# Kernel optimization log

Measured on AMD Instinct MI355X. Metric: run time of the kernel, lower is better.

## Reference

```python
import jax, jax.numpy as jnp
import numpy as np

D_INNER = 5120
DT_RANK = 160
N_STATE = 16
BATCH = 256


def _softplus_thresh20(x):
    # ttnn.softplus(parameter1=1.0, parameter2=20.0): linear above threshold 20
    return jnp.where(x > 20.0, x, jnp.log1p(jnp.exp(jnp.minimum(x, 20.0))))


def setup_inputs() -> dict:
    key = jax.random.key(0)
    ks = jax.random.split(key, 9)
    x = jax.random.normal(ks[0], (1, 1, BATCH, D_INNER), dtype=jnp.float32)
    # scale weights by 1/sqrt(fan_in) so softplus input is O(1)
    W_dt_low = jax.random.normal(ks[1], (D_INNER, DT_RANK), dtype=jnp.float32) / np.sqrt(D_INNER)
    W_dt = jax.random.normal(ks[2], (DT_RANK, D_INNER), dtype=jnp.float32) / np.sqrt(DT_RANK)
    b_dt = jax.random.normal(ks[3], (D_INNER,), dtype=jnp.float32)
    W_B = jax.random.normal(ks[4], (D_INNER, N_STATE), dtype=jnp.float32) / np.sqrt(D_INNER)
    W_C = jax.random.normal(ks[5], (D_INNER, N_STATE), dtype=jnp.float32) / np.sqrt(D_INNER)
    # A = -exp(A_log): strictly negative, as in the module's preprocess_A
    A = -jnp.exp(0.5 * jax.random.normal(ks[6], (D_INNER, N_STATE), dtype=jnp.float32))
    D = jax.random.normal(ks[7], (D_INNER,), dtype=jnp.float32)
    h0 = 0.1 * jax.random.normal(ks[8], (BATCH, D_INNER, N_STATE), dtype=jnp.float32)
    return {"x": x, "W_dt_low": W_dt_low, "W_dt": W_dt, "b_dt": b_dt,
            "W_B": W_B, "W_C": W_C, "A": A, "D": D, "h0": h0}


def reference(x, W_dt_low, W_dt, b_dt, W_B, W_C, A, D, h0):
    b, d = x.shape[2], x.shape[3]
    xb = x.reshape(b, d)                                  # (B, D)
    # delta = softplus(x @ x_proj_dt @ dt_proj + bias)
    delta = _softplus_thresh20(xb @ W_dt_low @ W_dt + b_dt)   # (B, D)
    Bp = xb @ W_B                                         # (B, N)
    Cp = xb @ W_C                                         # (B, N)
    # discretize: abar = exp(delta * A), bbar = delta * B
    # layout (B, D, N) matches repeat_interleave(delta, n) / repeat(B, d)
    abar = jnp.exp(delta[:, :, None] * A[None, :, :])     # (B, D, N)
    bbar = delta[:, :, None] * Bp[:, None, :]             # (B, D, N)
    h = abar * h0 + bbar * xb[:, :, None]                 # (B, D, N)
    y = jnp.einsum('bdn,bn->bd', h, Cp)                   # reduce over state
    out = xb * D[None, :] + y                             # (B, D)
    return out.reshape(1, 1, b, d)
```

## Files before the change

kernel.cpp:

```cpp
#include <hip/hip_runtime.h>
#include <math.h>

#define D_INNER 5120
#define DT_RANK 160
#define N_STATE 16
#define BATCH   256
#define KTOT    192

#define BGRP    8
#define NBG     (BATCH / BGRP)
#define DDBLK   160
#define NDDB    (D_INNER / DDBLK)
#define SPLIT   32

#define OFF_T     0
#define SZ_T      (BATCH * KTOT)
#define OFF_P     (OFF_T + SZ_T)
#define SZ_P      (SPLIT * BATCH * KTOT)
#define OFF_DELTA OFF_P

__global__ __launch_bounds__(256) void k1_gemm(const float* __restrict__ x,
                                               const float* __restrict__ Wdtlow,
                                               const float* __restrict__ WB,
                                               const float* __restrict__ WC,
                                               float* __restrict__ ws) {
    __shared__ float lds[4 * BGRP * KTOT];
    const int tid  = threadIdx.x;
    const int lane = tid & 63;
    const int wv   = tid >> 6;
    const int b0   = blockIdx.x * BGRP;
    const int ddB  = blockIdx.y * DDBLK;

    float* xs = lds;
    for (int j = tid; j < (BGRP * DDBLK) / 4; j += 256) {
        int i  = j / (DDBLK / 4);
        int c4 = j % (DDBLK / 4);
        float4 v = *(const float4*)(x + (size_t)(b0 + i) * D_INNER + ddB + c4 * 4);
        *(float4*)(xs + i * DDBLK + c4 * 4) = v;
    }
    __syncthreads();

    const int dd0 = wv * 40;
    const float* p0 = Wdtlow + (size_t)(ddB + dd0) * DT_RANK + lane;
    const float* p1 = p0 + 64;
    const float* p2;
    int st2;
    if (lane < 32)      { p2 = p0 + 128;                                          st2 = DT_RANK; }
    else if (lane < 48) { p2 = WB + (size_t)(ddB + dd0) * N_STATE + (lane - 32);  st2 = N_STATE; }
    else                { p2 = WC + (size_t)(ddB + dd0) * N_STATE + (lane - 48);  st2 = N_STATE; }

    float acc0[BGRP], acc1[BGRP], acc2[BGRP];
#pragma unroll
    for (int i = 0; i < BGRP; ++i) { acc0[i] = 0.f; acc1[i] = 0.f; acc2[i] = 0.f; }

#pragma unroll 2
    for (int g = 0; g < 10; ++g) {
        float w0[4], w1[4], w2[4];
#pragma unroll
        for (int u = 0; u < 4; ++u) {
            int dd = g * 4 + u;
            w0[u] = p0[(size_t)dd * DT_RANK];
            w1[u] = p1[(size_t)dd * DT_RANK];
            w2[u] = p2[(size_t)dd * st2];
        }
#pragma unroll
        for (int i = 0; i < BGRP; ++i) {
            float4 xv = *(const float4*)(xs + i * DDBLK + dd0 + g * 4);
            acc0[i] += xv.x * w0[0] + xv.y * w0[1] + xv.z * w0[2] + xv.w * w0[3];
            acc1[i] += xv.x * w1[0] + xv.y * w1[1] + xv.z * w1[2] + xv.w * w1[3];
            acc2[i] += xv.x * w2[0] + xv.y * w2[1] + xv.z * w2[2] + xv.w * w2[3];
        }
    }
    __syncthreads();

#pragma unroll
    for (int i = 0; i < BGRP; ++i) {
        float* r = lds + wv * (BGRP * KTOT) + i * KTOT;
        r[lane]       = acc0[i];
        r[lane + 64]  = acc1[i];
        r[lane + 128] = acc2[i];
    }
    __syncthreads();

    float* P = ws + OFF_P + (size_t)blockIdx.y * (BATCH * KTOT) + (size_t)b0 * KTOT;
#pragma unroll
    for (int r = 0; r < 6; ++r) {
        int idx = tid + r * 256;
        float v = lds[idx] + lds[idx + 1536] + lds[idx + 3072] + lds[idx + 4608];
        P[idx] = v;
    }
}

__global__ __launch_bounds__(256) void k2_reduce(float* __restrict__ ws) {
    int g = blockIdx.x * 256 + threadIdx.x;
    const float* P = ws + OFF_P;
    float a = 0.f;
#pragma unroll
    for (int s = 0; s < SPLIT; ++s) a += P[(size_t)s * (BATCH * KTOT) + g];
    ws[OFF_T + g] = a;
}

#define K3A_BT 8
__global__ __launch_bounds__(256) void k3a_delta(const float* __restrict__ Wdt,
                                                 const float* __restrict__ b_dt,
                                                 float* __restrict__ ws) {
    __shared__ float ts[DT_RANK * K3A_BT];
    const int tid = threadIdx.x;
    const int d   = blockIdx.x * 256 + tid;
    const int b0  = blockIdx.y * K3A_BT;
    const float* T = ws + OFF_T;

    for (int j = tid; j < DT_RANK * K3A_BT; j += 256) {
        int b = j & (K3A_BT - 1);
        int k = j >> 3;
        ts[j] = T[(size_t)(b0 + b) * KTOT + k];
    }
    __syncthreads();

    float acc[K3A_BT];
#pragma unroll
    for (int i = 0; i < K3A_BT; ++i) acc[i] = 0.f;

#pragma unroll 4
    for (int k = 0; k < DT_RANK; ++k) {
        float w = Wdt[(size_t)k * D_INNER + d];
        float4 t0 = *(const float4*)(ts + k * 8);
        float4 t1 = *(const float4*)(ts + k * 8 + 4);
        acc[0] += t0.x * w; acc[1] += t0.y * w; acc[2] += t0.z * w; acc[3] += t0.w * w;
        acc[4] += t1.x * w; acc[5] += t1.y * w; acc[6] += t1.z * w; acc[7] += t1.w * w;
    }

    const float bv = b_dt[d];
    float* delta = ws + OFF_DELTA;
#pragma unroll
    for (int i = 0; i < K3A_BT; ++i) {
        float v  = acc[i] + bv;
        float dl = (v > 20.f) ? v : log1pf(__expf(v));
        delta[(size_t)(b0 + i) * D_INNER + d] = dl;
    }
}

__global__ __launch_bounds__(256) void k3b_scan(const float* __restrict__ x,
                                                const float* __restrict__ A,
                                                const float* __restrict__ Dv,
                                                const float* __restrict__ h0,
                                                const float* __restrict__ ws,
                                                float* __restrict__ out) {
    const int tid  = threadIdx.x;
    const int dsub = tid >> 2;
    const int nq   = tid & 3;
    const int d    = blockIdx.x * 64 + dsub;
    const int b    = blockIdx.y;

    const float* Tb = ws + OFF_T + (size_t)b * KTOT;
    float sbc = 0.f;
#pragma unroll
    for (int n = 0; n < N_STATE; ++n) sbc += Tb[160 + n] * Tb[176 + n];
    float cp0 = Tb[176 + nq * 4 + 0];
    float cp1 = Tb[176 + nq * 4 + 1];
    float cp2 = Tb[176 + nq * 4 + 2];
    float cp3 = Tb[176 + nq * 4 + 3];

    const float delta = ws[OFF_DELTA + (size_t)b * D_INNER + d];
    float4 a = ((const float4*)(A + (size_t)d * N_STATE))[nq];
    float4 h = ((const float4*)(h0 + ((size_t)b * D_INNER + d) * N_STATE))[nq];

    float y = __expf(delta * a.x) * h.x * cp0
            + __expf(delta * a.y) * h.y * cp1
            + __expf(delta * a.z) * h.z * cp2
            + __expf(delta * a.w) * h.w * cp3;
    y += __shfl_xor(y, 1);
    y += __shfl_xor(y, 2);

    if (nq == 0) {
        float xv = x[(size_t)b * D_INNER + d];
        out[(size_t)b * D_INNER + d] = xv * (Dv[d] + delta * sbc) + y;
    }
}

extern "C" void kernel_launch(void* const* d_in, const int* in_sizes, int n_in,
                              void* d_out, int out_size, void* d_ws, size_t ws_size,
                              hipStream_t stream) {
    const float* x      = (const float*)d_in[0];
    const float* Wdtlow = (const float*)d_in[1];
    const float* Wdt    = (const float*)d_in[2];
    const float* bdt    = (const float*)d_in[3];
    const float* WB     = (const float*)d_in[4];
    const float* WC     = (const float*)d_in[5];
    const float* A      = (const float*)d_in[6];
    const float* Dv     = (const float*)d_in[7];
    const float* h0     = (const float*)d_in[8];
    float* ws  = (float*)d_ws;
    float* out = (float*)d_out;

    hipLaunchKernelGGL(k1_gemm, dim3(NBG, NDDB), dim3(256), 0, stream,
                       x, Wdtlow, WB, WC, ws);
    hipLaunchKernelGGL(k2_reduce, dim3((BATCH * KTOT) / 256), dim3(256), 0, stream, ws);
    hipLaunchKernelGGL(k3a_delta, dim3(D_INNER / 256, BATCH / K3A_BT), dim3(256),
                       0, stream, Wdt, bdt, ws);
    hipLaunchKernelGGL(k3b_scan, dim3(D_INNER / 64, BATCH), dim3(256), 0, stream,
                       x, A, Dv, h0, ws, out);
}
```

Before: 190.1 us.

## Fuse delta projection kernel with state reduction kernel

Merges the delta GEMM plus softplus kernel and the per-(b,d) state reduction kernel into one launch. Delta stays in registers, and each thread handles all 16 states for 8 batch rows, reusing A across those rows. This drops the delta workspace round trip and one launch. In exchange, h0 loads become per-thread 64-byte strided accesses with lower occupancy (640 blocks), which may reduce achieved bandwidth on the dominant h0 stream.

```diff
diff --git a/kernel.cpp b/kernel.cpp
--- a/kernel.cpp
+++ b/kernel.cpp
@@ -13,11 +13,12 @@
 #define NDDB    (D_INNER / DDBLK)
 #define SPLIT   32
 
+#define K3_BT   8
+
 #define OFF_T     0
 #define SZ_T      (BATCH * KTOT)
 #define OFF_P     (OFF_T + SZ_T)
 #define SZ_P      (SPLIT * BATCH * KTOT)
-#define OFF_DELTA OFF_P
 
 __global__ __launch_bounds__(256) void k1_gemm(const float* __restrict__ x,
                                                const float* __restrict__ Wdtlow,
@@ -86,8 +87,7 @@
 #pragma unroll
     for (int r = 0; r < 6; ++r) {
         int idx = tid + r * 256;
-        float v = lds[idx] + lds[idx + 1536] + lds[idx + 3072] + lds[idx + 4608];
-        P[idx] = v;
+        P[idx] = lds[idx] + lds[idx + 1536] + lds[idx + 3072] + lds[idx + 4608];
     }
 }
 
@@ -100,26 +100,30 @@
     ws[OFF_T + g] = a;
 }
 
-#define K3A_BT 8
-__global__ __launch_bounds__(256) void k3a_delta(const float* __restrict__ Wdt,
-                                                 const float* __restrict__ b_dt,
-                                                 float* __restrict__ ws) {
-    __shared__ float ts[DT_RANK * K3A_BT];
+__global__ __launch_bounds__(256) void k3_fused(const float* __restrict__ Wdt,
+                                                const float* __restrict__ b_dt,
+                                                const float* __restrict__ x,
+                                                const float* __restrict__ A,
+                                                const float* __restrict__ Dv,
+                                                const float* __restrict__ h0,
+                                                const float* __restrict__ ws,
+                                                float* __restrict__ out) {
+    __shared__ float ts[DT_RANK * K3_BT];
     const int tid = threadIdx.x;
     const int d   = blockIdx.x * 256 + tid;
-    const int b0  = blockIdx.y * K3A_BT;
+    const int b0  = blockIdx.y * K3_BT;
     const float* T = ws + OFF_T;
 
-    for (int j = tid; j < DT_RANK * K3A_BT; j += 256) {
-        int b = j & (K3A_BT - 1);
+    for (int j = tid; j < DT_RANK * K3_BT; j += 256) {
+        int b = j & (K3_BT - 1);
         int k = j >> 3;
         ts[j] = T[(size_t)(b0 + b) * KTOT + k];
     }
     __syncthreads();
 
-    float acc[K3A_BT];
+    float acc[K3_BT];
 #pragma unroll
-    for (int i = 0; i < K3A_BT; ++i) acc[i] = 0.f;
+    for (int i = 0; i < K3_BT; ++i) acc[i] = 0.f;
 
 #pragma unroll 4
     for (int k = 0; k < DT_RANK; ++k) {
@@ -131,50 +135,44 @@
     }
 
     const float bv = b_dt[d];
-    float* delta = ws + OFF_DELTA;
+    const float Dd = Dv[d];
+    const float4* a4 = (const float4*)(A + (size_t)d * N_STATE);
+    float4 a0 = a4[0], a1 = a4[1], a2 = a4[2], a3 = a4[3];
+
 #pragma unroll
-    for (int i = 0; i < K3A_BT; ++i) {
-        float v  = acc[i] + bv;
-        float dl = (v > 20.f) ? v : log1pf(__expf(v));
-        delta[(size_t)(b0 + i) * D_INNER + d] = dl;
-    }
-}
+    for (int i = 0; i < K3_BT; ++i) {
+        const int b = b0 + i;
+        float v     = acc[i] + bv;
+        float delta = (v > 20.f) ? v : log1pf(__expf(v));
 
-__global__ __launch_bounds__(256) void k3b_scan(const float* __restrict__ x,
-                                                const float* __restrict__ A,
-                                                const float* __restrict__ Dv,
-                                                const float* __restrict__ h0,
-                                                const float* __restrict__ ws,
-                                                float* __restrict__ out) {
-    const int tid  = threadIdx.x;
-    const int dsub = tid >> 2;
-    const int nq   = tid & 3;
-    const int d    = blockIdx.x * 64 + dsub;
-    const int b    = blockIdx.y;
+        const float* Tb = T + (size_t)b * KTOT;
+        float sbc = 0.f;
+#pragma unroll
+        for (int n = 0; n < N_STATE; ++n) sbc += Tb[160 + n] * Tb[176 + n];
 
-    const float* Tb = ws + OFF_T + (size_t)b * KTOT;
-    float sbc = 0.f;
-#pragma unroll
-    for (int n = 0; n < N_STATE; ++n) sbc += Tb[160 + n] * Tb[176 + n];
-    float cp0 = Tb[176 + nq * 4 + 0];
-    float cp1 = Tb[176 + nq * 4 + 1];
-    float cp2 = Tb[176 + nq * 4 + 2];
-    float cp3 = Tb[176 + nq * 4 + 3];
+        const float4* h4 = (const float4*)(h0 + ((size_t)b * D_INNER + d) * N_STATE);
+        float4 h_0 = h4[0], h_1 = h4[1], h_2 = h4[2], h_3 = h4[3];
 
-    const float delta = ws[OFF_DELTA + (size_t)b * D_INNER + d];
-    float4 a = ((const float4*)(A + (size_t)d * N_STATE))[nq];
-    float4 h = ((const float4*)(h0 + ((size_t)b * D_INNER + d) * N_STATE))[nq];
+        float y = 0.f;
+        y += __expf(delta * a0.x) * h_0.x * Tb[176 + 0];
+        y += __expf(delta * a0.y) * h_0.y * Tb[176 + 1];
+        y += __expf(delta * a0.z) * h_0.z * Tb[176 + 2];
+        y += __expf(delta * a0.w) * h_0.w * Tb[176 + 3];
+        y += __expf(delta * a1.x) * h_1.x * Tb[176 + 4];
+        y += __expf(delta * a1.y) * h_1.y * Tb[176 + 5];
+        y += __expf(delta * a1.z) * h_1.z * Tb[176 + 6];
+        y += __expf(delta * a1.w) * h_1.w * Tb[176 + 7];
+        y += __expf(delta * a2.x) * h_2.x * Tb[176 + 8];
+        y += __expf(delta * a2.y) * h_2.y * Tb[176 + 9];
+        y += __expf(delta * a2.z) * h_2.z * Tb[176 + 10];
+        y += __expf(delta * a2.w) * h_2.w * Tb[176 + 11];
+        y += __expf(delta * a3.x) * h_3.x * Tb[176 + 12];
+        y += __expf(delta * a3.y) * h_3.y * Tb[176 + 13];
+        y += __expf(delta * a3.z) * h_3.z * Tb[176 + 14];
+        y += __expf(delta * a3.w) * h_3.w * Tb[176 + 15];
 
-    float y = __expf(delta * a.x) * h.x * cp0
-            + __expf(delta * a.y) * h.y * cp1
-            + __expf(delta * a.z) * h.z * cp2
-            + __expf(delta * a.w) * h.w * cp3;
-    y += __shfl_xor(y, 1);
-    y += __shfl_xor(y, 2);
-
-    if (nq == 0) {
         float xv = x[(size_t)b * D_INNER + d];
-        out[(size_t)b * D_INNER + d] = xv * (Dv[d] + delta * sbc) + y;
+        out[(size_t)b * D_INNER + d] = xv * (Dd + delta * sbc) + y;
     }
 }
 
@@ -196,8 +194,6 @@
     hipLaunchKernelGGL(k1_gemm, dim3(NBG, NDDB), dim3(256), 0, stream,
                        x, Wdtlow, WB, WC, ws);
     hipLaunchKernelGGL(k2_reduce, dim3((BATCH * KTOT) / 256), dim3(256), 0, stream, ws);
-    hipLaunchKernelGGL(k3a_delta, dim3(D_INNER / 256, BATCH / K3A_BT), dim3(256),
-                       0, stream, Wdt, bdt, ws);
-    hipLaunchKernelGGL(k3b_scan, dim3(D_INNER / 64, BATCH), dim3(256), 0, stream,
-                       x, A, Dv, h0, ws, out);
+    hipLaunchKernelGGL(k3_fused, dim3(D_INNER / 256, BATCH / K3_BT), dim3(256),
+                       0, stream, Wdt, bdt, x, A, Dv, h0, ws, out);
 }
```

Result: faster. 183.1 us (-3.7%).
